# Performance work log

Hardware: AMD Instinct MI355X
Metric: run time of the kernel (lower is better)

## Reference

```python
import jax, jax.numpy as jnp
import numpy as np

N, E, IN, H, D = 50000, 800000, 16, 4, 64


def _gat_layer(x, W, a_s, a_d, b, src, dst, heads, concat):
    n = x.shape[0]
    h = (x @ W).reshape(n, heads, -1)                 # [N,H,D]
    es = jnp.einsum('nhd,hd->nh', h, a_s)             # alpha_src per node
    ed = jnp.einsum('nhd,hd->nh', h, a_d)             # alpha_dst per node
    e = jax.nn.leaky_relu(es[src] + ed[dst], 0.2)     # [E,H]
    # segment softmax over incoming edges of each dst node
    m = jax.ops.segment_max(e, dst, num_segments=n)
    ex = jnp.exp(e - m[dst])
    den = jax.ops.segment_sum(ex, dst, num_segments=n)
    alpha = ex / den[dst]                             # [E,H]
    out = jax.ops.segment_sum(h[src] * alpha[:, :, None], dst, num_segments=n)
    out = out.reshape(n, -1) if concat else out.mean(axis=1)
    return out + b


def setup_inputs() -> dict:
    key = jax.random.key(0)
    ks = jax.random.split(key, 16)
    x = jax.random.normal(ks[0], (N, IN), dtype=jnp.float32)
    edge_index = jax.random.randint(ks[1], (2, E), 0, N, dtype=jnp.int32)

    def lin(k, fi, fo):
        return jax.random.normal(k, (fi, fo), dtype=jnp.float32) / np.sqrt(fi)

    def att(k, heads, d):
        return jax.random.normal(k, (heads, d), dtype=jnp.float32) / np.sqrt(d)

    return dict(
        x=x, edge_index=edge_index,
        W1=lin(ks[2], IN, H * D), a1s=att(ks[3], H, D), a1d=att(ks[4], H, D),
        b1=jnp.zeros((H * D,), jnp.float32),
        W2=lin(ks[5], H * D, H * D), a2s=att(ks[6], H, D), a2d=att(ks[7], H, D),
        b2=jnp.zeros((H * D,), jnp.float32),
        W3=lin(ks[8], H * D, D), a3s=att(ks[9], 1, D), a3d=att(ks[10], 1, D),
        b3=jnp.zeros((D,), jnp.float32),
    )


def reference(x, edge_index, W1, a1s, a1d, b1, W2, a2s, a2d, b2, W3, a3s, a3d, b3):
    n = x.shape[0]
    loop = jnp.arange(n, dtype=edge_index.dtype)  # PyG GATConv adds self-loops
    src = jnp.concatenate([edge_index[0], loop])
    dst = jnp.concatenate([edge_index[1], loop])
    h = jax.nn.elu(_gat_layer(x, W1, a1s, a1d, b1, src, dst, H, True))
    h = jax.nn.elu(_gat_layer(h, W2, a2s, a2d, b2, src, dst, H, True))
    node_emb = _gat_layer(h, W3, a3s, a3d, b3, src, dst, 1, False)  # [N,64]
    graph_emb = node_emb.mean(axis=0, keepdims=True)                # [1,64]
    return node_emb, graph_emb
```

## Files before the change

### kernel.cpp

```cpp
#include <hip/hip_runtime.h>
#include <math.h>

#define NNODES 50000

typedef __attribute__((ext_vector_type(8))) short short8;
typedef __attribute__((ext_vector_type(4))) float f32x4;

__device__ __forceinline__ unsigned short f2bf(float f) {
    unsigned u = __float_as_uint(f);
    u += 0x7fffu + ((u >> 16) & 1);
    return (unsigned short)(u >> 16);
}
__device__ __forceinline__ float bf2f(unsigned short h) {
    return __uint_as_float(((unsigned)h) << 16);
}
__device__ __forceinline__ float bflo(unsigned u) { return __uint_as_float(u << 16); }
__device__ __forceinline__ float bfhi(unsigned u) { return __uint_as_float(u & 0xffff0000u); }

__global__ __launch_bounds__(256) void deg_init_kernel(int* __restrict__ deg, int N) {
    int i = blockIdx.x * 256 + threadIdx.x;
    if (i < N) deg[i] = 1;
}

__global__ __launch_bounds__(256) void deg_count_kernel(const int* __restrict__ ei,
                                                        int* __restrict__ deg, int E) {
    int i = blockIdx.x * 256 + threadIdx.x;
    if (i < E) atomicAdd(&deg[ei[E + i]], 1);
}

__global__ __launch_bounds__(256) void scan_partial_kernel(const int* __restrict__ deg,
                                                           int* __restrict__ bsum, int N) {
    __shared__ int ls[256];
    int t = threadIdx.x;
    int i = blockIdx.x * 256 + t;
    ls[t] = (i < N) ? deg[i] : 0;
    __syncthreads();
    #pragma unroll
    for (int off = 128; off; off >>= 1) {
        if (t < off) ls[t] += ls[t + off];
        __syncthreads();
    }
    if (t == 0) bsum[blockIdx.x] = ls[0];
}

__global__ __launch_bounds__(256) void scan_blocks_kernel(const int* __restrict__ bsum,
                                                          int* __restrict__ boff,
                                                          int* __restrict__ rowptrN, int nblk) {
    __shared__ int ls[256];
    int t = threadIdx.x;
    int v = (t < nblk) ? bsum[t] : 0;
    ls[t] = v;
    __syncthreads();
    for (int off = 1; off < 256; off <<= 1) {
        int u = (t >= off) ? ls[t - off] : 0;
        __syncthreads();
        ls[t] += u;
        __syncthreads();
    }
    if (t < nblk) boff[t] = ls[t] - v;
    if (t == 255) *rowptrN = ls[255];
}

__global__ __launch_bounds__(256) void scan_final_kernel(const int* __restrict__ deg,
                                                         const int* __restrict__ boff,
                                                         int* __restrict__ rowptr,
                                                         int* __restrict__ fill, int N) {
    __shared__ int ls[256];
    int t = threadIdx.x;
    int i = blockIdx.x * 256 + t;
    int v = (i < N) ? deg[i] : 0;
    ls[t] = v;
    __syncthreads();
    for (int off = 1; off < 256; off <<= 1) {
        int u = (t >= off) ? ls[t - off] : 0;
        __syncthreads();
        ls[t] += u;
        __syncthreads();
    }
    if (i < N) {
        int e = boff[blockIdx.x] + ls[t] - v;
        rowptr[i] = e;
        fill[i] = e;
    }
}

__global__ __launch_bounds__(256) void scatter_kernel(const int* __restrict__ ei,
                                                      int* __restrict__ fill,
                                                      int* __restrict__ col, int E, int N) {
    int i = blockIdx.x * 256 + threadIdx.x;
    int total = E + N;
    if (i >= total) return;
    int s, d;
    if (i < E) { s = ei[i]; d = ei[E + i]; }
    else       { s = i - E; d = s; }
    int pos = atomicAdd(&fill[d], 1);
    col[pos] = s;
}

__global__ __launch_bounds__(256) void w2t_prep_kernel(const float* __restrict__ W,
                                                       unsigned short* __restrict__ Th,
                                                       unsigned short* __restrict__ Tl) {
    int k = blockIdx.x, n = threadIdx.x;
    float w = W[k * 256 + n];
    unsigned short h = f2bf(w);
    unsigned short l = f2bf(w - bf2f(h));
    Th[n * 256 + k] = h;
    Tl[n * 256 + k] = l;
}

__global__ __launch_bounds__(256) void w3t_prep_kernel(const float* __restrict__ W,
                                                       unsigned short* __restrict__ Th,
                                                       unsigned short* __restrict__ Tl) {
    int n = blockIdx.x, k = threadIdx.x;
    float w = W[k * 64 + n];
    unsigned short h = f2bf(w);
    unsigned short l = f2bf(w - bf2f(h));
    Th[n * 256 + k] = h;
    Tl[n * 256 + k] = l;
}

#define LDK 40

__global__ __launch_bounds__(256) void gemm2_mfma_kernel(const unsigned short* __restrict__ Ahb,
                                                         const unsigned short* __restrict__ Alb,
                                                         const unsigned short* __restrict__ WTh,
                                                         const unsigned short* __restrict__ WTl,
                                                         unsigned short* __restrict__ Cb,
                                                         const float* __restrict__ as_,
                                                         const float* __restrict__ ad_,
                                                         float* __restrict__ es,
                                                         float* __restrict__ ed,
                                                         int M) {
    __shared__ __align__(16) unsigned short Ah[128][LDK], Al[128][LDK];
    __shared__ __align__(16) unsigned short Bh[128][LDK], Bl[128][LDK];
    int tid  = threadIdx.x;
    int lane = tid & 63, wave = tid >> 6;
    int wm = wave >> 1, wn = wave & 1;
    int bm = blockIdx.x * 128;
    int bn = blockIdx.y * 128;
    int c = lane & 15, q = lane >> 4;

    f32x4 acc[4][4] = {};

    for (int k0 = 0; k0 < 256; k0 += 32) {
        #pragma unroll
        for (int p = 0; p < 2; ++p) {
            int idx = p * 256 + tid;
            int r   = idx >> 2;
            int kc  = (idx & 3) * 8;
            int grow = bm + r;
            size_t go = (size_t)grow * 256 + k0 + kc;
            uint4 vh = make_uint4(0u,0u,0u,0u), vl = make_uint4(0u,0u,0u,0u);
            if (grow < M) {
                vh = *reinterpret_cast<const uint4*>(Ahb + go);
                vl = *reinterpret_cast<const uint4*>(Alb + go);
            }
            *reinterpret_cast<uint4*>(&Ah[r][kc]) = vh;
            *reinterpret_cast<uint4*>(&Al[r][kc]) = vl;
        }
        #pragma unroll
        for (int p = 0; p < 2; ++p) {
            int idx = p * 256 + tid;
            int n   = idx >> 2;
            int kc  = (idx & 3) * 8;
            const size_t go = (size_t)(bn + n) * 256 + k0 + kc;
            *reinterpret_cast<uint4*>(&Bh[n][kc]) = *reinterpret_cast<const uint4*>(WTh + go);
            *reinterpret_cast<uint4*>(&Bl[n][kc]) = *reinterpret_cast<const uint4*>(WTl + go);
        }
        __syncthreads();

        short8 bh[4], bl[4];
        #pragma unroll
        for (int nt = 0; nt < 4; ++nt) {
            bh[nt] = *reinterpret_cast<const short8*>(&Bh[wn * 64 + nt * 16 + c][q * 8]);
            bl[nt] = *reinterpret_cast<const short8*>(&Bl[wn * 64 + nt * 16 + c][q * 8]);
        }
        #pragma unroll
        for (int mt = 0; mt < 4; ++mt) {
            short8 ah = *reinterpret_cast<const short8*>(&Ah[wm * 64 + mt * 16 + c][q * 8]);
            short8 al = *reinterpret_cast<const short8*>(&Al[wm * 64 + mt * 16 + c][q * 8]);
            #pragma unroll
            for (int nt = 0; nt < 4; ++nt) {
                acc[mt][nt] = __builtin_amdgcn_mfma_f32_16x16x32_bf16(ah, bh[nt], acc[mt][nt], 0, 0, 0);
                acc[mt][nt] = __builtin_amdgcn_mfma_f32_16x16x32_bf16(ah, bl[nt], acc[mt][nt], 0, 0, 0);
                acc[mt][nt] = __builtin_amdgcn_mfma_f32_16x16x32_bf16(al, bh[nt], acc[mt][nt], 0, 0, 0);
            }
        }
        __syncthreads();
    }

    #pragma unroll
    for (int mt = 0; mt < 4; ++mt) {
        #pragma unroll
        for (int r = 0; r < 4; ++r) {
            int gr = bm + wm * 64 + mt * 16 + q * 4 + r;
            if (gr < M) {
                #pragma unroll
                for (int nt = 0; nt < 4; ++nt) {
                    Cb[(size_t)gr * 256 + bn + wn * 64 + nt * 16 + c] = f2bf(acc[mt][nt][r]);
                }
            }
        }
    }
    int head = blockIdx.y * 2 + wn;
    float asv[4], adv[4];
    #pragma unroll
    for (int nt = 0; nt < 4; ++nt) {
        asv[nt] = as_[head * 64 + nt * 16 + c];
        adv[nt] = ad_[head * 64 + nt * 16 + c];
    }
    #pragma unroll
    for (int mt = 0; mt < 4; ++mt) {
        #pragma unroll
        for (int r = 0; r < 4; ++r) {
            float s = 0.f, d = 0.f;
            #pragma unroll
            for (int nt = 0; nt < 4; ++nt) {
                s += acc[mt][nt][r] * asv[nt];
                d += acc[mt][nt][r] * adv[nt];
            }
            #pragma unroll
            for (int off = 1; off < 16; off <<= 1) {
                s += __shfl_xor(s, off, 64);
                d += __shfl_xor(d, off, 64);
            }
            int gr = bm + wm * 64 + mt * 16 + q * 4 + r;
            if (c == 0 && gr < M) {
                es[(size_t)gr * 4 + head] = s;
                ed[(size_t)gr * 4 + head] = d;
            }
        }
    }
}

__global__ __launch_bounds__(256) void gemm3_mfma_kernel(const unsigned short* __restrict__ Ab,
                                                         const unsigned short* __restrict__ WTh,
                                                         const unsigned short* __restrict__ WTl,
                                                         unsigned short* __restrict__ Cb,
                                                         const float* __restrict__ as_,
                                                         const float* __restrict__ ad_,
                                                         float* __restrict__ es,
                                                         float* __restrict__ ed,
                                                         int M) {
    __shared__ __align__(16) unsigned short Ah[128][LDK];
    __shared__ __align__(16) unsigned short Bh[64][LDK], Bl[64][LDK];
    int tid = threadIdx.x, lane = tid & 63, wave = tid >> 6;
    int bm = blockIdx.x * 128;
    int c = lane & 15, q = lane >> 4;
    f32x4 acc[2][4] = {};

    for (int k0 = 0; k0 < 256; k0 += 32) {
        #pragma unroll
        for (int p = 0; p < 2; ++p) {
            int idx = p * 256 + tid;
            int r   = idx >> 2;
            int kf  = (idx & 3) * 8;
            int grow = bm + r;
            uint4 v = (grow < M)
                ? *reinterpret_cast<const uint4*>(Ab + (size_t)grow * 256 + k0 + kf)
                : make_uint4(0u, 0u, 0u, 0u);
            *reinterpret_cast<uint4*>(&Ah[r][kf]) = v;
        }
        {
            int n  = tid >> 2;
            int kc = (tid & 3) * 8;
            size_t go = (size_t)n * 256 + k0 + kc;
            *reinterpret_cast<uint4*>(&Bh[n][kc]) = *reinterpret_cast<const uint4*>(WTh + go);
            *reinterpret_cast<uint4*>(&Bl[n][kc]) = *reinterpret_cast<const uint4*>(WTl + go);
        }
        __syncthreads();

        short8 bh[4], bl[4];
        #pragma unroll
        for (int nt = 0; nt < 4; ++nt) {
            bh[nt] = *reinterpret_cast<const short8*>(&Bh[nt * 16 + c][q * 8]);
            bl[nt] = *reinterpret_cast<const short8*>(&Bl[nt * 16 + c][q * 8]);
        }
        #pragma unroll
        for (int mt = 0; mt < 2; ++mt) {
            short8 a = *reinterpret_cast<const short8*>(&Ah[wave * 32 + mt * 16 + c][q * 8]);
            #pragma unroll
            for (int nt = 0; nt < 4; ++nt) {
                acc[mt][nt] = __builtin_amdgcn_mfma_f32_16x16x32_bf16(a, bh[nt], acc[mt][nt], 0, 0, 0);
                acc[mt][nt] = __builtin_amdgcn_mfma_f32_16x16x32_bf16(a, bl[nt], acc[mt][nt], 0, 0, 0);
            }
        }
        __syncthreads();
    }

    float asv[4], adv[4];
    #pragma unroll
    for (int nt = 0; nt < 4; ++nt) { asv[nt] = as_[nt * 16 + c]; adv[nt] = ad_[nt * 16 + c]; }
    #pragma unroll
    for (int mt = 0; mt < 2; ++mt) {
        #pragma unroll
        for (int r = 0; r < 4; ++r) {
            int gr = bm + wave * 32 + mt * 16 + q * 4 + r;
            bool ok = gr < M;
            if (ok) {
                #pragma unroll
                for (int nt = 0; nt < 4; ++nt)
                    Cb[(size_t)gr * 64 + nt * 16 + c] = f2bf(acc[mt][nt][r]);
            }
            float s = 0.f, d = 0.f;
            #pragma unroll
            for (int nt = 0; nt < 4; ++nt) {
                s += acc[mt][nt][r] * asv[nt];
                d += acc[mt][nt][r] * adv[nt];
            }
            #pragma unroll
            for (int off = 1; off < 16; off <<= 1) {
                s += __shfl_xor(s, off, 64);
                d += __shfl_xor(d, off, 64);
            }
            if (c == 0 && ok) { es[gr] = s; ed[gr] = d; }
        }
    }
}

template <int H>
__global__ __launch_bounds__(256) void gemm_attn_kernel(const float* __restrict__ A,
                                                        const float* __restrict__ B,
                                                        unsigned short* __restrict__ Cb,
                                                        const float* __restrict__ as_,
                                                        const float* __restrict__ ad_,
                                                        float* __restrict__ es,
                                                        float* __restrict__ ed,
                                                        int M, int K, int Ncol) {
    __shared__ __align__(16) float As[16][64];
    __shared__ __align__(16) float Bs[16][64];
    int tid = threadIdx.x;
    int bm = blockIdx.x * 64;
    int bn = blockIdx.y * 64;
    int tm = (tid >> 4) * 4;
    int tn = (tid & 15) * 4;
    float acc[4][4] = {};
    int ar  = tid >> 2;
    int akk = (tid & 3) * 4;
    int brr = tid >> 4;
    int bcc = (tid & 15) * 4;
    for (int k0 = 0; k0 < K; k0 += 16) {
        int grow = bm + ar;
        float4 av;
        if (grow < M) av = *reinterpret_cast<const float4*>(A + (size_t)grow * K + k0 + akk);
        else          av = make_float4(0.f, 0.f, 0.f, 0.f);
        As[akk + 0][ar] = av.x;
        As[akk + 1][ar] = av.y;
        As[akk + 2][ar] = av.z;
        As[akk + 3][ar] = av.w;
        float4 bv = *reinterpret_cast<const float4*>(B + (size_t)(k0 + brr) * Ncol + bn + bcc);
        *reinterpret_cast<float4*>(&Bs[brr][bcc]) = bv;
        __syncthreads();
        #pragma unroll
        for (int kk = 0; kk < 16; ++kk) {
            float4 a4 = *reinterpret_cast<const float4*>(&As[kk][tm]);
            float4 b4 = *reinterpret_cast<const float4*>(&Bs[kk][tn]);
            float a[4] = {a4.x, a4.y, a4.z, a4.w};
            float b[4] = {b4.x, b4.y, b4.z, b4.w};
            #pragma unroll
            for (int i = 0; i < 4; ++i)
                #pragma unroll
                for (int j = 0; j < 4; ++j) acc[i][j] += a[i] * b[j];
        }
        __syncthreads();
    }
    #pragma unroll
    for (int i = 0; i < 4; ++i) {
        int gr = bm + tm + i;
        if (gr < M) {
            ushort4 r;
            r.x = f2bf(acc[i][0]); r.y = f2bf(acc[i][1]);
            r.z = f2bf(acc[i][2]); r.w = f2bf(acc[i][3]);
            *reinterpret_cast<ushort4*>(Cb + (size_t)gr * Ncol + bn + tn) = r;
        }
    }
    int hy = blockIdx.y;
    float4 asv = *reinterpret_cast<const float4*>(as_ + (size_t)hy * 64 + tn);
    float4 adv = *reinterpret_cast<const float4*>(ad_ + (size_t)hy * 64 + tn);
    float sv[4], dv[4];
    #pragma unroll
    for (int i = 0; i < 4; ++i) {
        sv[i] = acc[i][0] * asv.x + acc[i][1] * asv.y + acc[i][2] * asv.z + acc[i][3] * asv.w;
        dv[i] = acc[i][0] * adv.x + acc[i][1] * adv.y + acc[i][2] * adv.z + acc[i][3] * adv.w;
    }
    #pragma unroll
    for (int off = 1; off < 16; off <<= 1) {
        #pragma unroll
        for (int i = 0; i < 4; ++i) {
            sv[i] += __shfl_xor(sv[i], off, 64);
            dv[i] += __shfl_xor(dv[i], off, 64);
        }
    }
    if ((tid & 15) == 0) {
        #pragma unroll
        for (int i = 0; i < 4; ++i) {
            int gr = bm + tm + i;
            if (gr < M) {
                es[(size_t)gr * H + hy] = sv[i];
                ed[(size_t)gr * H + hy] = dv[i];
            }
        }
    }
}

__device__ __forceinline__ float lrelu02(float x) { return x > 0.f ? x : 0.2f * x; }
__device__ __forceinline__ float eluf(float x)    { return x > 0.f ? x : expm1f(x); }

template <int ACT, int OUTMODE>
__global__ __launch_bounds__(256) void agg4_kernel(const unsigned short* __restrict__ hb,
                                                   const float* __restrict__ es,
                                                   const float* __restrict__ ed,
                                                   const int* __restrict__ rowptr,
                                                   const int* __restrict__ col,
                                                   const float* __restrict__ bias,
                                                   void* __restrict__ outp,
                                                   void* __restrict__ outp2, int N) {
    __shared__ int   slds[4][64];
    __shared__ float plds[4][4][68];
    int sub  = threadIdx.x >> 6;
    int lane = threadIdx.x & 63;
    int node = blockIdx.x * 4 + sub;
    if (node >= N) return;
    int s = rowptr[node], t = rowptr[node + 1];

    float edv[4];
    #pragma unroll
    for (int h = 0; h < 4; ++h) edv[h] = ed[(size_t)node * 4 + h];

    int half = lane >> 5, sl = lane & 31;
    int hh8 = sl >> 3;
    float den[4] = {0.f, 0.f, 0.f, 0.f};
    float4 a0 = make_float4(0.f, 0.f, 0.f, 0.f);
    float4 a1 = make_float4(0.f, 0.f, 0.f, 0.f);

    for (int base = s; base < t; base += 64) {
        int j = base + lane;
        int m = t - base; if (m > 64) m = 64;
        int sc = 0;
        float p[4] = {0.f, 0.f, 0.f, 0.f};
        if (j < t) {
            sc = col[j];
            float4 e4 = *reinterpret_cast<const float4*>(es + (size_t)sc * 4);
            p[0] = __expf(lrelu02(e4.x + edv[0]));
            p[1] = __expf(lrelu02(e4.y + edv[1]));
            p[2] = __expf(lrelu02(e4.z + edv[2]));
            p[3] = __expf(lrelu02(e4.w + edv[3]));
        }
        slds[sub][lane] = sc;
        #pragma unroll
        for (int h = 0; h < 4; ++h) {
            den[h] += p[h];
            plds[sub][h][lane] = p[h];
        }
        int nit = (m + 1) >> 1;
        #pragma unroll 4
        for (int it = 0; it < nit; ++it) {
            int idx = 2 * it + half;
            int scj = slds[sub][idx];
            float a = plds[sub][hh8][idx];
            uint4 u = *reinterpret_cast<const uint4*>(hb + (size_t)scj * 256 + sl * 8);
            a0.x += bflo(u.x) * a;
            a0.y += bfhi(u.x) * a;
            a0.z += bflo(u.y) * a;
            a0.w += bfhi(u.y) * a;
            a1.x += bflo(u.z) * a;
            a1.y += bfhi(u.z) * a;
            a1.z += bflo(u.w) * a;
            a1.w += bfhi(u.w) * a;
        }
    }
    a0.x += __shfl_xor(a0.x, 32, 64);
    a0.y += __shfl_xor(a0.y, 32, 64);
    a0.z += __shfl_xor(a0.z, 32, 64);
    a0.w += __shfl_xor(a0.w, 32, 64);
    a1.x += __shfl_xor(a1.x, 32, 64);
    a1.y += __shfl_xor(a1.y, 32, 64);
    a1.z += __shfl_xor(a1.z, 32, 64);
    a1.w += __shfl_xor(a1.w, 32, 64);
    #pragma unroll
    for (int off = 32; off; off >>= 1)
        #pragma unroll
        for (int h = 0; h < 4; ++h) den[h] += __shfl_xor(den[h], off, 64);

    if (half == 0) {
        float inv = 1.f / den[hh8];
        float4 bv0 = *reinterpret_cast<const float4*>(bias + sl * 8);
        float4 bv1 = *reinterpret_cast<const float4*>(bias + sl * 8 + 4);
        float r[8];
        r[0] = a0.x * inv + bv0.x; r[1] = a0.y * inv + bv0.y;
        r[2] = a0.z * inv + bv0.z; r[3] = a0.w * inv + bv0.w;
        r[4] = a1.x * inv + bv1.x; r[5] = a1.y * inv + bv1.y;
        r[6] = a1.z * inv + bv1.z; r[7] = a1.w * inv + bv1.w;
        if (ACT) {
            #pragma unroll
            for (int e = 0; e < 8; ++e) r[e] = eluf(r[e]);
        }
        if constexpr (OUTMODE == 0) {
            float* o = (float*)outp + (size_t)node * 256 + sl * 8;
            *reinterpret_cast<float4*>(o)     = make_float4(r[0], r[1], r[2], r[3]);
            *reinterpret_cast<float4*>(o + 4) = make_float4(r[4], r[5], r[6], r[7]);
        } else if constexpr (OUTMODE == 1) {
            unsigned short ob[8];
            #pragma unroll
            for (int e = 0; e < 8; ++e) ob[e] = f2bf(r[e]);
            *reinterpret_cast<uint4*>((unsigned short*)outp + (size_t)node * 256 + sl * 8) =
                *reinterpret_cast<const uint4*>(ob);
        } else {
            unsigned short oh[8], ol[8];
            #pragma unroll
            for (int e = 0; e < 8; ++e) {
                oh[e] = f2bf(r[e]);
                ol[e] = f2bf(r[e] - bf2f(oh[e]));
            }
            size_t o = (size_t)node * 256 + sl * 8;
            *reinterpret_cast<uint4*>((unsigned short*)outp  + o) = *reinterpret_cast<const uint4*>(oh);
            *reinterpret_cast<uint4*>((unsigned short*)outp2 + o) = *reinterpret_cast<const uint4*>(ol);
        }
    }
}

__global__ __launch_bounds__(256) void agg1_kernel(const unsigned short* __restrict__ hb,
                                                   const float* __restrict__ es,
                                                   const float* __restrict__ ed,
                                                   const int* __restrict__ rowptr,
                                                   const int* __restrict__ col,
                                                   const float* __restrict__ bias,
                                                   float* __restrict__ out, int N) {
    __shared__ int   slds[4][64];
    __shared__ float plds[4][64];
    int sub  = threadIdx.x >> 6;
    int lane = threadIdx.x & 63;
    int node = blockIdx.x * 4 + sub;
    if (node >= N) return;
    int s = rowptr[node], t = rowptr[node + 1];
    float edv = ed[node];

    float den = 0.f, acc = 0.f;
    for (int base = s; base < t; base += 64) {
        int j = base + lane;
        int m = t - base; if (m > 64) m = 64;
        int sc = 0;
        float p0 = 0.f;
        if (j < t) {
            sc = col[j];
            p0 = __expf(lrelu02(es[sc] + edv));
        }
        slds[sub][lane] = sc;
        plds[sub][lane] = p0;
        den += p0;
        #pragma unroll 4
        for (int jj = 0; jj < m; ++jj) {
            int scj = slds[sub][jj];
            float a = plds[sub][jj];
            acc += bf2f(hb[(size_t)scj * 64 + lane]) * a;
        }
    }
    #pragma unroll
    for (int off = 32; off; off >>= 1) den += __shfl_xor(den, off, 64);
    out[(size_t)node * 64 + lane] = acc * (1.f / den) + bias[lane];
}

__global__ __launch_bounds__(256) void gmean_partial(const float* __restrict__ ne,
                                                     float* __restrict__ part, int N) {
    int d = threadIdx.x & 63, sub = threadIdx.x >> 6;
    int start = blockIdx.x * 4 + sub;
    float s = 0.f;
    for (int n = start; n < N; n += gridDim.x * 4) s += ne[(size_t)n * 64 + d];
    __shared__ float ls[256];
    ls[threadIdx.x] = s;
    __syncthreads();
    if (threadIdx.x < 64) {
        float v = ls[threadIdx.x] + ls[threadIdx.x + 64] + ls[threadIdx.x + 128] + ls[threadIdx.x + 192];
        part[blockIdx.x * 64 + d] = v;
    }
}

__global__ __launch_bounds__(64) void gmean_final(const float* __restrict__ part,
                                                  float* __restrict__ gout, int nblk, float invN) {
    int d = threadIdx.x;
    float s = 0.f;
    for (int b = 0; b < nblk; ++b) s += part[b * 64 + d];
    gout[d] = s * invN;
}

extern "C" void kernel_launch(void* const* d_in, const int* in_sizes, int n_in,
                              void* d_out, int out_size, void* d_ws, size_t ws_size,
                              hipStream_t stream) {
    const float* x   = (const float*)d_in[0];
    const int*   ei  = (const int*)d_in[1];
    const float* W1  = (const float*)d_in[2];
    const float* a1s = (const float*)d_in[3];
    const float* a1d = (const float*)d_in[4];
    const float* b1  = (const float*)d_in[5];
    const float* W2  = (const float*)d_in[6];
    const float* a2s = (const float*)d_in[7];
    const float* a2d = (const float*)d_in[8];
    const float* b2  = (const float*)d_in[9];
    const float* W3  = (const float*)d_in[10];
    const float* a3s = (const float*)d_in[11];
    const float* a3d = (const float*)d_in[12];
    const float* b3  = (const float*)d_in[13];
    float* out = (float*)d_out;

    const int N = NNODES;
    const int E = in_sizes[1] / 2;
    const int NB = (N + 255) / 256;

    char* w = (char*)d_ws;
    unsigned short* Hb   = (unsigned short*)w; w += (size_t)N * 256 * 2;
    unsigned short* B0b  = (unsigned short*)w; w += (size_t)N * 256 * 2;
    unsigned short* H3b  = (unsigned short*)w; w += (size_t)N * 64 * 2;
    unsigned short* A1h  = (unsigned short*)w; w += (size_t)N * 256 * 2;
    unsigned short* A1l  = (unsigned short*)w; w += (size_t)N * 256 * 2;
    float* es = (float*)w; w += (size_t)N * 4 * 4;
    float* ed = (float*)w; w += (size_t)N * 4 * 4;
    unsigned short* W2Th = (unsigned short*)w; w += 256 * 256 * 2;
    unsigned short* W2Tl = (unsigned short*)w; w += 256 * 256 * 2;
    unsigned short* W3Th = (unsigned short*)w; w += 64 * 256 * 2;
    unsigned short* W3Tl = (unsigned short*)w; w += 64 * 256 * 2;
    int* deg    = (int*)w; w += (size_t)N * 4;
    int* rowptr = (int*)w; w += (size_t)(N + 2) * 4;
    int* fill   = (int*)w; w += (size_t)N * 4;
    int* col    = (int*)w; w += (size_t)(E + N) * 4;
    int* bsum   = (int*)w; w += 256 * 4;
    int* boff   = (int*)w; w += 256 * 4;
    float* part = (float*)w; w += 128 * 64 * 4;
    (void)ws_size; (void)n_in; (void)out_size;

    deg_init_kernel<<<NB, 256, 0, stream>>>(deg, N);
    deg_count_kernel<<<(E + 255) / 256, 256, 0, stream>>>(ei, deg, E);
    scan_partial_kernel<<<NB, 256, 0, stream>>>(deg, bsum, N);
    scan_blocks_kernel<<<1, 256, 0, stream>>>(bsum, boff, rowptr + N, NB);
    scan_final_kernel<<<NB, 256, 0, stream>>>(deg, boff, rowptr, fill, N);
    scatter_kernel<<<(E + N + 255) / 256, 256, 0, stream>>>(ei, fill, col, E, N);
    w2t_prep_kernel<<<256, 256, 0, stream>>>(W2, W2Th, W2Tl);
    w3t_prep_kernel<<<64, 256, 0, stream>>>(W3, W3Th, W3Tl);

    gemm_attn_kernel<4><<<dim3((N + 63) / 64, 4), 256, 0, stream>>>(
        x, W1, Hb, a1s, a1d, es, ed, N, 16, 256);
    agg4_kernel<1, 2><<<(N + 3) / 4, 256, 0, stream>>>(Hb, es, ed, rowptr, col, b1, A1h, A1l, N);

    gemm2_mfma_kernel<<<dim3((N + 127) / 128, 2), 256, 0, stream>>>(
        A1h, A1l, W2Th, W2Tl, Hb, a2s, a2d, es, ed, N);
    agg4_kernel<1, 1><<<(N + 3) / 4, 256, 0, stream>>>(Hb, es, ed, rowptr, col, b2, B0b, nullptr, N);

    gemm3_mfma_kernel<<<(N + 127) / 128, 256, 0, stream>>>(
        B0b, W3Th, W3Tl, H3b, a3s, a3d, es, ed, N);
    agg1_kernel<<<(N + 3) / 4, 256, 0, stream>>>(H3b, es, ed, rowptr, col, b3, out, N);

    gmean_partial<<<128, 256, 0, stream>>>(out, part, N);
    gmean_final<<<1, 64, 0, stream>>>(part, out + (size_t)N * 64, 128, 1.0f / N);
}
```

Before: 467.4 us.

## Retune gather widths in aggregation kernels and merge weight-prep launches

In the 4-head aggregation kernel, each lane now walks every edge with an 8-byte load of 4 features, where before the wave was split into two halves that each took alternate edges with 16-byte loads followed by a cross-half shuffle reduction. The 1-head aggregation kernel goes the other way: it switches to half-wave edge splitting with 4-byte paired loads. The degree-init kernel becomes a memset, with the self-loop +1 folded into the scan, and the two weight-prep kernels are merged into one launch. These changes trade per-edge load width against loop trip count and launch overhead, and the mixed directions make the net effect unclear.

```diff
diff --git a/kernel.cpp b/kernel.cpp
--- a/kernel.cpp
+++ b/kernel.cpp
@@ -16,11 +16,6 @@
 }
 __device__ __forceinline__ float bflo(unsigned u) { return __uint_as_float(u << 16); }
 __device__ __forceinline__ float bfhi(unsigned u) { return __uint_as_float(u & 0xffff0000u); }
-
-__global__ __launch_bounds__(256) void deg_init_kernel(int* __restrict__ deg, int N) {
-    int i = blockIdx.x * 256 + threadIdx.x;
-    if (i < N) deg[i] = 1;
-}
 
 __global__ __launch_bounds__(256) void deg_count_kernel(const int* __restrict__ ei,
                                                         int* __restrict__ deg, int E) {
@@ -33,7 +28,7 @@
     __shared__ int ls[256];
     int t = threadIdx.x;
     int i = blockIdx.x * 256 + t;
-    ls[t] = (i < N) ? deg[i] : 0;
+    ls[t] = (i < N) ? deg[i] + 1 : 0;
     __syncthreads();
     #pragma unroll
     for (int off = 128; off; off >>= 1) {
@@ -68,7 +63,7 @@
     __shared__ int ls[256];
     int t = threadIdx.x;
     int i = blockIdx.x * 256 + t;
-    int v = (i < N) ? deg[i] : 0;
+    int v = (i < N) ? deg[i] + 1 : 0;
     ls[t] = v;
     __syncthreads();
     for (int off = 1; off < 256; off <<= 1) {
@@ -97,26 +92,28 @@
     col[pos] = s;
 }
 
-__global__ __launch_bounds__(256) void w2t_prep_kernel(const float* __restrict__ W,
-                                                       unsigned short* __restrict__ Th,
-                                                       unsigned short* __restrict__ Tl) {
-    int k = blockIdx.x, n = threadIdx.x;
-    float w = W[k * 256 + n];
-    unsigned short h = f2bf(w);
-    unsigned short l = f2bf(w - bf2f(h));
-    Th[n * 256 + k] = h;
-    Tl[n * 256 + k] = l;
-}
-
-__global__ __launch_bounds__(256) void w3t_prep_kernel(const float* __restrict__ W,
-                                                       unsigned short* __restrict__ Th,
-                                                       unsigned short* __restrict__ Tl) {
-    int n = blockIdx.x, k = threadIdx.x;
-    float w = W[k * 64 + n];
-    unsigned short h = f2bf(w);
-    unsigned short l = f2bf(w - bf2f(h));
-    Th[n * 256 + k] = h;
-    Tl[n * 256 + k] = l;
+__global__ __launch_bounds__(256) void wprep_kernel(const float* __restrict__ W2,
+                                                    const float* __restrict__ W3,
+                                                    unsigned short* __restrict__ W2Th,
+                                                    unsigned short* __restrict__ W2Tl,
+                                                    unsigned short* __restrict__ W3Th,
+                                                    unsigned short* __restrict__ W3Tl) {
+    int b = blockIdx.x;
+    if (b < 256) {
+        int k = b, n = threadIdx.x;
+        float w = W2[k * 256 + n];
+        unsigned short h = f2bf(w);
+        unsigned short l = f2bf(w - bf2f(h));
+        W2Th[n * 256 + k] = h;
+        W2Tl[n * 256 + k] = l;
+    } else {
+        int n = b - 256, k = threadIdx.x;
+        float w = W3[k * 64 + n];
+        unsigned short h = f2bf(w);
+        unsigned short l = f2bf(w - bf2f(h));
+        W3Th[n * 256 + k] = h;
+        W3Tl[n * 256 + k] = l;
+    }
 }
 
 #define LDK 40
@@ -427,12 +424,9 @@
     #pragma unroll
     for (int h = 0; h < 4; ++h) edv[h] = ed[(size_t)node * 4 + h];
 
-    int half = lane >> 5, sl = lane & 31;
-    int hh8 = sl >> 3;
     float den[4] = {0.f, 0.f, 0.f, 0.f};
-    float4 a0 = make_float4(0.f, 0.f, 0.f, 0.f);
-    float4 a1 = make_float4(0.f, 0.f, 0.f, 0.f);
-
+    int hh = lane >> 4;
+    float4 acc = make_float4(0.f, 0.f, 0.f, 0.f);
     for (int base = s; base < t; base += 64) {
         int j = base + lane;
         int m = t - base; if (m > 64) m = 64;
@@ -452,70 +446,44 @@
             den[h] += p[h];
             plds[sub][h][lane] = p[h];
         }
-        int nit = (m + 1) >> 1;
         #pragma unroll 4
-        for (int it = 0; it < nit; ++it) {
-            int idx = 2 * it + half;
-            int scj = slds[sub][idx];
-            float a = plds[sub][hh8][idx];
-            uint4 u = *reinterpret_cast<const uint4*>(hb + (size_t)scj * 256 + sl * 8);
-            a0.x += bflo(u.x) * a;
-            a0.y += bfhi(u.x) * a;
-            a0.z += bflo(u.y) * a;
-            a0.w += bfhi(u.y) * a;
-            a1.x += bflo(u.z) * a;
-            a1.y += bfhi(u.z) * a;
-            a1.z += bflo(u.w) * a;
-            a1.w += bfhi(u.w) * a;
-        }
-    }
-    a0.x += __shfl_xor(a0.x, 32, 64);
-    a0.y += __shfl_xor(a0.y, 32, 64);
-    a0.z += __shfl_xor(a0.z, 32, 64);
-    a0.w += __shfl_xor(a0.w, 32, 64);
-    a1.x += __shfl_xor(a1.x, 32, 64);
-    a1.y += __shfl_xor(a1.y, 32, 64);
-    a1.z += __shfl_xor(a1.z, 32, 64);
-    a1.w += __shfl_xor(a1.w, 32, 64);
+        for (int jj = 0; jj < m; ++jj) {
+            int scj = slds[sub][jj];
+            float a = plds[sub][hh][jj];
+            uint2 u = *reinterpret_cast<const uint2*>(hb + (size_t)scj * 256 + lane * 4);
+            acc.x += bflo(u.x) * a;
+            acc.y += bfhi(u.x) * a;
+            acc.z += bflo(u.y) * a;
+            acc.w += bfhi(u.y) * a;
+        }
+    }
     #pragma unroll
     for (int off = 32; off; off >>= 1)
         #pragma unroll
         for (int h = 0; h < 4; ++h) den[h] += __shfl_xor(den[h], off, 64);
-
-    if (half == 0) {
-        float inv = 1.f / den[hh8];
-        float4 bv0 = *reinterpret_cast<const float4*>(bias + sl * 8);
-        float4 bv1 = *reinterpret_cast<const float4*>(bias + sl * 8 + 4);
-        float r[8];
-        r[0] = a0.x * inv + bv0.x; r[1] = a0.y * inv + bv0.y;
-        r[2] = a0.z * inv + bv0.z; r[3] = a0.w * inv + bv0.w;
-        r[4] = a1.x * inv + bv1.x; r[5] = a1.y * inv + bv1.y;
-        r[6] = a1.z * inv + bv1.z; r[7] = a1.w * inv + bv1.w;
-        if (ACT) {
-            #pragma unroll
-            for (int e = 0; e < 8; ++e) r[e] = eluf(r[e]);
-        }
-        if constexpr (OUTMODE == 0) {
-            float* o = (float*)outp + (size_t)node * 256 + sl * 8;
-            *reinterpret_cast<float4*>(o)     = make_float4(r[0], r[1], r[2], r[3]);
-            *reinterpret_cast<float4*>(o + 4) = make_float4(r[4], r[5], r[6], r[7]);
-        } else if constexpr (OUTMODE == 1) {
-            unsigned short ob[8];
-            #pragma unroll
-            for (int e = 0; e < 8; ++e) ob[e] = f2bf(r[e]);
-            *reinterpret_cast<uint4*>((unsigned short*)outp + (size_t)node * 256 + sl * 8) =
-                *reinterpret_cast<const uint4*>(ob);
-        } else {
-            unsigned short oh[8], ol[8];
-            #pragma unroll
-            for (int e = 0; e < 8; ++e) {
-                oh[e] = f2bf(r[e]);
-                ol[e] = f2bf(r[e] - bf2f(oh[e]));
-            }
-            size_t o = (size_t)node * 256 + sl * 8;
-            *reinterpret_cast<uint4*>((unsigned short*)outp  + o) = *reinterpret_cast<const uint4*>(oh);
-            *reinterpret_cast<uint4*>((unsigned short*)outp2 + o) = *reinterpret_cast<const uint4*>(ol);
-        }
+    float inv = 1.f / den[hh];
+    float4 bv = *reinterpret_cast<const float4*>(bias + lane * 4);
+    float r0 = acc.x * inv + bv.x;
+    float r1 = acc.y * inv + bv.y;
+    float r2 = acc.z * inv + bv.z;
+    float r3 = acc.w * inv + bv.w;
+    if (ACT) { r0 = eluf(r0); r1 = eluf(r1); r2 = eluf(r2); r3 = eluf(r3); }
+    if constexpr (OUTMODE == 0) {
+        *reinterpret_cast<float4*>((float*)outp + (size_t)node * 256 + lane * 4) =
+            make_float4(r0, r1, r2, r3);
+    } else if constexpr (OUTMODE == 1) {
+        ushort4 o;
+        o.x = f2bf(r0); o.y = f2bf(r1); o.z = f2bf(r2); o.w = f2bf(r3);
+        *reinterpret_cast<ushort4*>((unsigned short*)outp + (size_t)node * 256 + lane * 4) = o;
+    } else {
+        ushort4 oh, ol;
+        oh.x = f2bf(r0); ol.x = f2bf(r0 - bf2f(oh.x));
+        oh.y = f2bf(r1); ol.y = f2bf(r1 - bf2f(oh.y));
+        oh.z = f2bf(r2); ol.z = f2bf(r2 - bf2f(oh.z));
+        oh.w = f2bf(r3); ol.w = f2bf(r3 - bf2f(oh.w));
+        size_t o = (size_t)node * 256 + lane * 4;
+        *reinterpret_cast<ushort4*>((unsigned short*)outp  + o) = oh;
+        *reinterpret_cast<ushort4*>((unsigned short*)outp2 + o) = ol;
     }
 }
 
@@ -535,7 +503,8 @@
     int s = rowptr[node], t = rowptr[node + 1];
     float edv = ed[node];
 
-    float den = 0.f, acc = 0.f;
+    int half = lane >> 5, sl = lane & 31;
+    float den = 0.f, acc0 = 0.f, acc1 = 0.f;
     for (int base = s; base < t; base += 64) {
         int j = base + lane;
         int m = t - base; if (m > 64) m = 64;
@@ -548,16 +517,27 @@
         slds[sub][lane] = sc;
         plds[sub][lane] = p0;
         den += p0;
+        int nit = (m + 1) >> 1;
         #pragma unroll 4
-        for (int jj = 0; jj < m; ++jj) {
-            int scj = slds[sub][jj];
-            float a = plds[sub][jj];
-            acc += bf2f(hb[(size_t)scj * 64 + lane]) * a;
-        }
-    }
+        for (int it = 0; it < nit; ++it) {
+            int idx = 2 * it + half;
+            int scj = slds[sub][idx];
+            float a = plds[sub][idx];
+            unsigned u = *reinterpret_cast<const unsigned*>(hb + (size_t)scj * 64 + sl * 2);
+            acc0 += bflo(u) * a;
+            acc1 += bfhi(u) * a;
+        }
+    }
+    acc0 += __shfl_xor(acc0, 32, 64);
+    acc1 += __shfl_xor(acc1, 32, 64);
     #pragma unroll
     for (int off = 32; off; off >>= 1) den += __shfl_xor(den, off, 64);
-    out[(size_t)node * 64 + lane] = acc * (1.f / den) + bias[lane];
+    if (half == 0) {
+        float inv = 1.f / den;
+        float2 b = *reinterpret_cast<const float2*>(bias + sl * 2);
+        *reinterpret_cast<float2*>(out + (size_t)node * 64 + sl * 2) =
+            make_float2(acc0 * inv + b.x, acc1 * inv + b.y);
+    }
 }
 
 __global__ __launch_bounds__(256) void gmean_partial(const float* __restrict__ ne,
@@ -627,14 +607,13 @@
     float* part = (float*)w; w += 128 * 64 * 4;
     (void)ws_size; (void)n_in; (void)out_size;
 
-    deg_init_kernel<<<NB, 256, 0, stream>>>(deg, N);
+    hipMemsetAsync(deg, 0, (size_t)N * 4, stream);
     deg_count_kernel<<<(E + 255) / 256, 256, 0, stream>>>(ei, deg, E);
     scan_partial_kernel<<<NB, 256, 0, stream>>>(deg, bsum, N);
     scan_blocks_kernel<<<1, 256, 0, stream>>>(bsum, boff, rowptr + N, NB);
     scan_final_kernel<<<NB, 256, 0, stream>>>(deg, boff, rowptr, fill, N);
     scatter_kernel<<<(E + N + 255) / 256, 256, 0, stream>>>(ei, fill, col, E, N);
-    w2t_prep_kernel<<<256, 256, 0, stream>>>(W2, W2Th, W2Tl);
-    w3t_prep_kernel<<<64, 256, 0, stream>>>(W3, W3Th, W3Tl);
+    wprep_kernel<<<320, 256, 0, stream>>>(W2, W3, W2Th, W2Tl, W3Th, W3Tl);
 
     gemm_attn_kernel<4><<<dim3((N + 63) / 64, 4), 256, 0, stream>>>(
         x, W1, Hb, a1s, a1d, es, ed, N, 16, 256);
```

After: 468.2 us. About the same (+0.2%).
